# Performance work log

Hardware: AMD Instinct MI355X
Metric: run time of the kernel (lower is better)

Reference implementation:

```python
import jax, jax.numpy as jnp
import numpy as np

H_IMG, W_IMG = 256, 512      # image_size
P = 224                      # focus_patch_size
FS = 14                      # feature_size -> L = 196
DM = 384                     # d_model
POOL = P // FS               # 16


def _grid_sample_bilinear_zeros(img, grid):
    """torch F.grid_sample(mode='bilinear', padding_mode='zeros', align_corners=False).
    img: (B, C, H, W), grid: (B, Ho, Wo, 2) with (x, y) in [-1, 1]. -> (B, C, Ho, Wo)"""
    B, C, H, W = img.shape
    ix = (grid[..., 0] + 1.0) * (W * 0.5) - 0.5
    iy = (grid[..., 1] + 1.0) * (H * 0.5) - 0.5
    x0 = jnp.floor(ix); y0 = jnp.floor(iy)
    x1 = x0 + 1.0;      y1 = y0 + 1.0
    wx1 = ix - x0; wx0 = 1.0 - wx1
    wy1 = iy - y0; wy0 = 1.0 - wy1

    def gather(im, yy, xx):
        valid = ((xx >= 0) & (xx < W) & (yy >= 0) & (yy < H)).astype(im.dtype)
        xc = jnp.clip(xx, 0, W - 1).astype(jnp.int32)
        yc = jnp.clip(yy, 0, H - 1).astype(jnp.int32)
        return im[:, yc, xc] * valid[None]  # (C, Ho, Wo)

    def sample_one(im, x0, x1, y0, y1, wx0, wx1, wy0, wy1):
        return (gather(im, y0, x0) * (wy0 * wx0)[None]
                + gather(im, y0, x1) * (wy0 * wx1)[None]
                + gather(im, y1, x0) * (wy1 * wx0)[None]
                + gather(im, y1, x1) * (wy1 * wx1)[None])

    return jax.vmap(sample_one)(img, x0, x1, y0, y1, wx0, wx1, wy0, wy1)


def setup_inputs() -> dict:
    key = jax.random.key(0)
    ks = jax.random.split(key, 9)
    B = 128
    images = jax.random.normal(ks[0], (B, 3, H_IMG, W_IMG), jnp.float32)
    positions = jax.random.uniform(ks[1], (B, 2), jnp.float32)          # (x, y) in [0,1]
    global_features = jax.random.normal(ks[2], (B, FS * FS, DM), jnp.float32)
    Wp = jax.random.normal(ks[3], (3, DM), jnp.float32) * 0.1           # focus_net stand-in proj
    bp = jnp.zeros((DM,), jnp.float32)
    w1 = jax.random.normal(ks[4], (DM, DM // 4), jnp.float32) * 0.05    # fusion-weight MLP
    b1 = jnp.zeros((DM // 4,), jnp.float32)
    w2 = jax.random.normal(ks[5], (DM // 4, 1), jnp.float32) * 0.05
    b2 = jnp.zeros((1,), jnp.float32)
    return dict(images=images, positions=positions, global_features=global_features,
                Wp=Wp, bp=bp, w1=w1, b1=b1, w2=w2, b2=b2, seq_len=1)


def reference(images, positions, global_features, Wp, bp, w1, b1, w2, b2, seq_len):
    B = images.shape[0]
    L = FS * FS
    # ---- get_img_patches: wraparound crop (vectorized over batch) ----
    px = jnp.clip(positions[:, 0], 0.0, 1.0)
    py = jnp.clip(positions[:, 1], 0.0, 1.0)
    x_start = (jnp.trunc(px * W_IMG - P / 2).astype(jnp.int32)) % W_IMG           # int() then % W
    y_start = jnp.floor(jnp.clip(py * H_IMG - P / 2, 0.0, H_IMG - P)).astype(jnp.int32)
    xi = (x_start[:, None] + jnp.arange(P)[None, :]) % W_IMG                      # (B, P) wraparound
    yi = y_start[:, None] + jnp.arange(P)[None, :]                                # (B, P)
    patches = jax.vmap(lambda im, y, x: im[:, y][:, :, x])(images, yi, xi)        # (B, 3, P, P)

    # affine_grid(theta, (1,1,FS,FS), align_corners=False)
    xs = x_start.astype(jnp.float32)
    ys = y_start.astype(jnp.float32)
    u = ((jnp.arange(FS, dtype=jnp.float32) + 0.5) * 2.0 / FS) - 1.0              # base grid coords
    gx = (P / W_IMG) * u[None, None, :] + ((2.0 * xs + P) / W_IMG - 1.0)[:, None, None]
    gy = (P / H_IMG) * u[None, :, None] + ((2.0 * ys + P) / H_IMG - 1.0)[:, None, None]
    grid = jnp.stack([jnp.broadcast_to(gx, (B, FS, FS)),
                      jnp.broadcast_to(gy, (B, FS, FS))], axis=-1)                # (B, FS, FS, 2)

    # ---- focus_net stand-in: 16x16 avg-pool + linear 3 -> d_model ----
    pooled = patches.reshape(B, 3, FS, POOL, FS, POOL).mean(axis=(3, 5))          # (B, 3, FS, FS)
    local = jnp.einsum('bchw,cd->bhwd', pooled, Wp) + bp                          # (B, FS, FS, DM)
    local_features = local.reshape(B, L, DM)

    # ---- update_global_features: grid_sample scatter + gated update ----
    local_2d = local.transpose(0, 3, 1, 2)                                        # (B, DM, FS, FS)
    fw = jax.nn.sigmoid(jnp.einsum('blk,ko->blo',
                                   jax.nn.gelu(jnp.einsum('blc,ch->blh', local_features, w1) + b1),
                                   w2) + b2)                                      # (B, L, 1)
    sampled = _grid_sample_bilinear_zeros(local_2d, grid)                         # (B, DM, FS, FS)
    sampled = sampled.transpose(0, 2, 3, 1).reshape(B, L, DM)
    updated = global_features + fw * sampled                                      # broadcast expand
    return updated
```

## Files before the change

kernel.cpp:

```cpp
#include <hip/hip_runtime.h>
#include <math.h>

#define H_IMG 256
#define W_IMG 512
#define PSZ   224
#define FS    14
#define L     196
#define DM    384
#define HID   96

__device__ __forceinline__ void get_starts(const float* __restrict__ pos, int b,
                                           int& xs, int& ys) {
    float px = pos[b * 2 + 0];
    float py = pos[b * 2 + 1];
    px = fminf(fmaxf(px, 0.0f), 1.0f);
    py = fminf(fmaxf(py, 0.0f), 1.0f);
    int xv = (int)truncf(px * (float)W_IMG - 112.0f);
    xs = ((xv % W_IMG) + W_IMG) % W_IMG;
    float yv = py * (float)H_IMG - 112.0f;
    yv = fminf(fmaxf(yv, 0.0f), (float)(H_IMG - PSZ));
    ys = (int)floorf(yv);
}

__global__ __launch_bounds__(256) void pool_kernel(const float* __restrict__ img,
                                                   const float* __restrict__ pos,
                                                   float* __restrict__ pooled,
                                                   int B) {
    int blk = blockIdx.x;
    int b = blk / FS;
    int i = blk % FS;
    int t = threadIdx.x;
    int xs, ys;
    get_starts(pos, b, xs, ys);
    if (t < PSZ) {
        int col = xs + t;
        if (col >= W_IMG) col -= W_IMG;
        int row0 = ys + i * 16;
        #pragma unroll
        for (int c = 0; c < 3; ++c) {
            const float* ip = img + ((size_t)(b * 3 + c) * H_IMG) * W_IMG;
            float acc = 0.0f;
            #pragma unroll
            for (int dy = 0; dy < 16; ++dy)
                acc += ip[(size_t)(row0 + dy) * W_IMG + col];
            acc += __shfl_xor(acc, 1);
            acc += __shfl_xor(acc, 2);
            acc += __shfl_xor(acc, 4);
            acc += __shfl_xor(acc, 8);
            if ((t & 15) == 0)
                pooled[(size_t)(b * 3 + c) * L + i * FS + (t >> 4)] = acc * (1.0f / 256.0f);
        }
    }
}

__global__ void precompute_kernel(const float* __restrict__ Wp, const float* __restrict__ bp,
                                  const float* __restrict__ w1, const float* __restrict__ b1,
                                  float* __restrict__ A, float* __restrict__ B0) {
    int k = threadIdx.x;
    if (k < HID) {
        float a0 = 0.f, a1 = 0.f, a2 = 0.f, ab = 0.f;
        for (int d = 0; d < DM; ++d) {
            float w = w1[d * HID + k];
            a0 += Wp[0 * DM + d] * w;
            a1 += Wp[1 * DM + d] * w;
            a2 += Wp[2 * DM + d] * w;
            ab += bp[d] * w;
        }
        A[0 * HID + k] = a0;
        A[1 * HID + k] = a1;
        A[2 * HID + k] = a2;
        B0[k] = ab + b1[k];
    }
}

__global__ __launch_bounds__(256) void fw_kernel(const float* __restrict__ pos,
                                                 const float* __restrict__ pooled,
                                                 const float* __restrict__ A,
                                                 const float* __restrict__ B0,
                                                 const float* __restrict__ w2,
                                                 const float* __restrict__ b2,
                                                 float4* __restrict__ metaA,
                                                 float* __restrict__ metaB,
                                                 int B) {
    __shared__ float sA[3 * HID];
    __shared__ float sB0[HID];
    __shared__ float sw2[HID];
    for (int k = threadIdx.x; k < 3 * HID; k += blockDim.x) sA[k] = A[k];
    for (int k = threadIdx.x; k < HID; k += blockDim.x) { sB0[k] = B0[k]; sw2[k] = w2[k]; }
    __syncthreads();

    int idx = blockIdx.x * blockDim.x + threadIdx.x;
    if (idx >= B * L) return;
    int b = idx / L;
    int l = idx % L;
    int i = l / FS;
    int j = l % FS;

    const float* pb = pooled + (size_t)b * 3 * L;
    float p0 = pb[l], p1 = pb[L + l], p2 = pb[2 * L + l];

    float s = 0.0f;
    for (int k = 0; k < HID; ++k) {
        float x = sB0[k] + p0 * sA[k] + p1 * sA[HID + k] + p2 * sA[2 * HID + k];
        float inner = 0.7978845608028654f * (x + 0.044715f * x * x * x);
        float g = 0.5f * x * (1.0f + tanhf(inner));
        s += g * sw2[k];
    }
    float fw = 1.0f / (1.0f + expf(-(s + b2[0])));

    int xs, ys;
    get_starts(pos, b, xs, ys);
    float uj = ((j + 0.5f) * 2.0f) / 14.0f - 1.0f;
    float ui = ((i + 0.5f) * 2.0f) / 14.0f - 1.0f;
    float gx = (224.0f / 512.0f) * uj + ((2.0f * (float)xs + 224.0f) / 512.0f - 1.0f);
    float gy = (224.0f / 256.0f) * ui + ((2.0f * (float)ys + 224.0f) / 256.0f - 1.0f);
    float ix = (gx + 1.0f) * 7.0f - 0.5f;
    float iy = (gy + 1.0f) * 7.0f - 0.5f;
    float x0f = floorf(ix), y0f = floorf(iy);
    float wx1 = ix - x0f, wx0 = 1.0f - wx1;
    float wy1 = iy - y0f, wy0 = 1.0f - wy1;
    int x0 = (int)x0f, y0 = (int)y0f;
    int x1 = x0 + 1, y1 = y0 + 1;

    float ps0 = 0.f, ps1 = 0.f, ps2 = 0.f, wsum = 0.f;
    const int   cx[4] = { x0, x1, x0, x1 };
    const int   cy[4] = { y0, y0, y1, y1 };
    const float cw[4] = { wy0 * wx0, wy0 * wx1, wy1 * wx0, wy1 * wx1 };
    #pragma unroll
    for (int n = 0; n < 4; ++n) {
        int X = cx[n], Y = cy[n];
        if (X >= 0 && X < FS && Y >= 0 && Y < FS) {
            float w = cw[n];
            int li = Y * FS + X;
            ps0 += w * pb[li];
            ps1 += w * pb[L + li];
            ps2 += w * pb[2 * L + li];
            wsum += w;
        }
    }
    metaA[idx] = make_float4(fw, wsum, ps0, ps1);
    metaB[idx] = ps2;
}

__global__ __launch_bounds__(256) void update_kernel(const float* __restrict__ gf,
                                                     const float* __restrict__ Wp,
                                                     const float* __restrict__ bp,
                                                     const float4* __restrict__ metaA,
                                                     const float* __restrict__ metaB,
                                                     float* __restrict__ out,
                                                     int total4) {
    int idx4 = blockIdx.x * blockDim.x + threadIdx.x;
    if (idx4 >= total4) return;
    int token = idx4 / (DM / 4);
    int d4 = idx4 % (DM / 4);

    float4 m = metaA[token];
    float ps2 = metaB[token];
    float fw = m.x, wsum = m.y, ps0 = m.z, ps1 = m.w;

    const float4* gf4 = (const float4*)gf;
    const float4* Wp4 = (const float4*)Wp;
    const float4* bp4 = (const float4*)bp;
    float4 g  = gf4[idx4];
    float4 w0 = Wp4[0 * (DM / 4) + d4];
    float4 w1v = Wp4[1 * (DM / 4) + d4];
    float4 w2v = Wp4[2 * (DM / 4) + d4];
    float4 bv = bp4[d4];

    float4 o;
    o.x = g.x + fw * (wsum * bv.x + ps0 * w0.x + ps1 * w1v.x + ps2 * w2v.x);
    o.y = g.y + fw * (wsum * bv.y + ps0 * w0.y + ps1 * w1v.y + ps2 * w2v.y);
    o.z = g.z + fw * (wsum * bv.z + ps0 * w0.z + ps1 * w1v.z + ps2 * w2v.z);
    o.w = g.w + fw * (wsum * bv.w + ps0 * w0.w + ps1 * w1v.w + ps2 * w2v.w);
    ((float4*)out)[idx4] = o;
}

extern "C" void kernel_launch(void* const* d_in, const int* in_sizes, int n_in,
                              void* d_out, int out_size, void* d_ws, size_t ws_size,
                              hipStream_t stream) {
    const float* images    = (const float*)d_in[0];
    const float* positions = (const float*)d_in[1];
    const float* gf        = (const float*)d_in[2];
    const float* Wp        = (const float*)d_in[3];
    const float* bp        = (const float*)d_in[4];
    const float* w1        = (const float*)d_in[5];
    const float* b1        = (const float*)d_in[6];
    const float* w2        = (const float*)d_in[7];
    const float* b2        = (const float*)d_in[8];

    const int B = in_sizes[1] / 2;

    float* ws = (float*)d_ws;
    float*  pooled = ws;
    float*  A      = ws + (size_t)B * 3 * L;
    float*  B0     = A + 3 * HID;
    float*  metaAf = B0 + HID;
    float4* metaA  = (float4*)metaAf;
    float*  metaB  = metaAf + (size_t)B * L * 4;

    hipLaunchKernelGGL(pool_kernel, dim3(B * FS), dim3(256), 0, stream,
                       images, positions, pooled, B);
    hipLaunchKernelGGL(precompute_kernel, dim3(1), dim3(128), 0, stream,
                       Wp, bp, w1, b1, A, B0);
    int tok = B * L;
    hipLaunchKernelGGL(fw_kernel, dim3((tok + 255) / 256), dim3(256), 0, stream,
                       positions, pooled, A, B0, w2, b2, metaA, metaB, B);
    int total4 = tok * (DM / 4);
    hipLaunchKernelGGL(update_kernel, dim3((total4 + 255) / 256), dim3(256), 0, stream,
                       gf, Wp, bp, metaA, metaB, (float*)d_out, total4);
}
```

Measured before the change: 65.16 us.

## Fuse pooling with weight precompute and fw computation with the update

Merges the four launches into two. The tiny weight precompute now runs inside block 0 of the pooling kernel, and the per-token gate/sampling computation is fused into the broadcast update kernel through shared-memory metadata, so the metaA/metaB round trip through global memory goes away. The gate MLP is split across 8 threads per token using a fast exp-based tanh, and Wp/bp are staged in shared memory. Pooling now accumulates all three channels in one loop. The fast-math tanh changes numerics slightly, and the gate work per block adds latency before the streaming phase.

Result: faster. 59.91 us (-8.1%).

```diff
diff --git a/kernel.cpp b/kernel.cpp
--- a/kernel.cpp
+++ b/kernel.cpp
@@ -8,6 +8,7 @@
 #define L     196
 #define DM    384
 #define HID   96
+#define TPB   32
 
 __device__ __forceinline__ void get_starts(const float* __restrict__ pos, int b,
                                            int& xs, int& ys) {
@@ -22,157 +23,178 @@
     ys = (int)floorf(yv);
 }
 
-__global__ __launch_bounds__(256) void pool_kernel(const float* __restrict__ img,
-                                                   const float* __restrict__ pos,
-                                                   float* __restrict__ pooled,
-                                                   int B) {
+__global__ __launch_bounds__(256) void pool_pre_kernel(
+    const float* __restrict__ img, const float* __restrict__ pos,
+    const float* __restrict__ Wp,  const float* __restrict__ bp,
+    const float* __restrict__ w1,  const float* __restrict__ b1,
+    float* __restrict__ pooled, float* __restrict__ A, float* __restrict__ B0,
+    int B)
+{
+    const int HW = H_IMG * W_IMG;
     int blk = blockIdx.x;
     int b = blk / FS;
     int i = blk % FS;
     int t = threadIdx.x;
     int xs, ys;
     get_starts(pos, b, xs, ys);
+
     if (t < PSZ) {
         int col = xs + t;
         if (col >= W_IMG) col -= W_IMG;
         int row0 = ys + i * 16;
+        const float* ip = img + (size_t)b * 3 * HW + (size_t)row0 * W_IMG + col;
+        float a0 = 0.f, a1 = 0.f, a2 = 0.f;
         #pragma unroll
-        for (int c = 0; c < 3; ++c) {
-            const float* ip = img + ((size_t)(b * 3 + c) * H_IMG) * W_IMG;
-            float acc = 0.0f;
-            #pragma unroll
-            for (int dy = 0; dy < 16; ++dy)
-                acc += ip[(size_t)(row0 + dy) * W_IMG + col];
-            acc += __shfl_xor(acc, 1);
-            acc += __shfl_xor(acc, 2);
-            acc += __shfl_xor(acc, 4);
-            acc += __shfl_xor(acc, 8);
-            if ((t & 15) == 0)
-                pooled[(size_t)(b * 3 + c) * L + i * FS + (t >> 4)] = acc * (1.0f / 256.0f);
-        }
-    }
-}
-
-__global__ void precompute_kernel(const float* __restrict__ Wp, const float* __restrict__ bp,
-                                  const float* __restrict__ w1, const float* __restrict__ b1,
-                                  float* __restrict__ A, float* __restrict__ B0) {
-    int k = threadIdx.x;
-    if (k < HID) {
+        for (int dy = 0; dy < 16; ++dy) {
+            const float* r = ip + dy * W_IMG;
+            a0 += r[0];
+            a1 += r[HW];
+            a2 += r[2 * HW];
+        }
+        #pragma unroll
+        for (int d = 1; d < 16; d <<= 1) {
+            a0 += __shfl_xor(a0, d);
+            a1 += __shfl_xor(a1, d);
+            a2 += __shfl_xor(a2, d);
+        }
+        if ((t & 15) == 0) {
+            int li = i * FS + (t >> 4);
+            pooled[((size_t)b * 3 + 0) * L + li] = a0 * (1.0f / 256.0f);
+            pooled[((size_t)b * 3 + 1) * L + li] = a1 * (1.0f / 256.0f);
+            pooled[((size_t)b * 3 + 2) * L + li] = a2 * (1.0f / 256.0f);
+        }
+    }
+
+    if (blk == 0 && t < HID) {
         float a0 = 0.f, a1 = 0.f, a2 = 0.f, ab = 0.f;
+        #pragma unroll 4
         for (int d = 0; d < DM; ++d) {
-            float w = w1[d * HID + k];
+            float w = w1[d * HID + t];
             a0 += Wp[0 * DM + d] * w;
             a1 += Wp[1 * DM + d] * w;
             a2 += Wp[2 * DM + d] * w;
             ab += bp[d] * w;
         }
-        A[0 * HID + k] = a0;
-        A[1 * HID + k] = a1;
-        A[2 * HID + k] = a2;
-        B0[k] = ab + b1[k];
-    }
-}
-
-__global__ __launch_bounds__(256) void fw_kernel(const float* __restrict__ pos,
-                                                 const float* __restrict__ pooled,
-                                                 const float* __restrict__ A,
-                                                 const float* __restrict__ B0,
-                                                 const float* __restrict__ w2,
-                                                 const float* __restrict__ b2,
-                                                 float4* __restrict__ metaA,
-                                                 float* __restrict__ metaB,
-                                                 int B) {
-    __shared__ float sA[3 * HID];
-    __shared__ float sB0[HID];
-    __shared__ float sw2[HID];
-    for (int k = threadIdx.x; k < 3 * HID; k += blockDim.x) sA[k] = A[k];
-    for (int k = threadIdx.x; k < HID; k += blockDim.x) { sB0[k] = B0[k]; sw2[k] = w2[k]; }
+        A[0 * HID + t] = a0;
+        A[1 * HID + t] = a1;
+        A[2 * HID + t] = a2;
+        B0[t] = ab + b1[t];
+    }
+}
+
+__global__ __launch_bounds__(256) void fused_update_kernel(
+    const float* __restrict__ pos, const float* __restrict__ pooled,
+    const float* __restrict__ A,   const float* __restrict__ B0,
+    const float* __restrict__ w2,  const float* __restrict__ b2,
+    const float* __restrict__ gf,  const float* __restrict__ Wp,
+    const float* __restrict__ bp,  float* __restrict__ out, int B)
+{
+    __shared__ float  sA[3 * HID];
+    __shared__ float  sB0[HID];
+    __shared__ float  sw2[HID];
+    __shared__ float4 sWp4[3 * DM / 4];
+    __shared__ float4 sbp4[DM / 4];
+    __shared__ float  sMeta[TPB][5];
+
+    int tid = threadIdx.x;
+    if (tid < 3 * HID) sA[tid] = A[tid];
+    if (tid < HID) { sB0[tid] = B0[tid]; sw2[tid] = w2[tid]; }
+    {
+        if (tid < 288) sWp4[tid] = ((const float4*)Wp)[tid];
+        if (tid < 96)  sbp4[tid] = ((const float4*)bp)[tid];
+    }
     __syncthreads();
 
-    int idx = blockIdx.x * blockDim.x + threadIdx.x;
-    if (idx >= B * L) return;
-    int b = idx / L;
-    int l = idx % L;
-    int i = l / FS;
-    int j = l % FS;
+    const int nTok = B * L;
+    int bt = blockIdx.x * TPB;
+    int g = tid >> 3;
+    int s = tid & 7;
+    int token = bt + g;
+    if (token >= nTok) token = nTok - 1;
+    int b = token / L;
+    int l = token % L;
 
     const float* pb = pooled + (size_t)b * 3 * L;
     float p0 = pb[l], p1 = pb[L + l], p2 = pb[2 * L + l];
 
-    float s = 0.0f;
-    for (int k = 0; k < HID; ++k) {
+    float acc = 0.0f;
+    #pragma unroll
+    for (int m = 0; m < 12; ++m) {
+        int k = s + 8 * m;
         float x = sB0[k] + p0 * sA[k] + p1 * sA[HID + k] + p2 * sA[2 * HID + k];
-        float inner = 0.7978845608028654f * (x + 0.044715f * x * x * x);
-        float g = 0.5f * x * (1.0f + tanhf(inner));
-        s += g * sw2[k];
-    }
-    float fw = 1.0f / (1.0f + expf(-(s + b2[0])));
-
-    int xs, ys;
-    get_starts(pos, b, xs, ys);
-    float uj = ((j + 0.5f) * 2.0f) / 14.0f - 1.0f;
-    float ui = ((i + 0.5f) * 2.0f) / 14.0f - 1.0f;
-    float gx = (224.0f / 512.0f) * uj + ((2.0f * (float)xs + 224.0f) / 512.0f - 1.0f);
-    float gy = (224.0f / 256.0f) * ui + ((2.0f * (float)ys + 224.0f) / 256.0f - 1.0f);
-    float ix = (gx + 1.0f) * 7.0f - 0.5f;
-    float iy = (gy + 1.0f) * 7.0f - 0.5f;
-    float x0f = floorf(ix), y0f = floorf(iy);
-    float wx1 = ix - x0f, wx0 = 1.0f - wx1;
-    float wy1 = iy - y0f, wy0 = 1.0f - wy1;
-    int x0 = (int)x0f, y0 = (int)y0f;
-    int x1 = x0 + 1, y1 = y0 + 1;
-
-    float ps0 = 0.f, ps1 = 0.f, ps2 = 0.f, wsum = 0.f;
-    const int   cx[4] = { x0, x1, x0, x1 };
-    const int   cy[4] = { y0, y0, y1, y1 };
-    const float cw[4] = { wy0 * wx0, wy0 * wx1, wy1 * wx0, wy1 * wx1 };
+        float e = __expf(1.5957691216057308f * (x + 0.044715f * x * x * x));
+        float th = 1.0f - 2.0f / (e + 1.0f);
+        acc += 0.5f * x * (1.0f + th) * sw2[k];
+    }
+    acc += __shfl_xor(acc, 1);
+    acc += __shfl_xor(acc, 2);
+    acc += __shfl_xor(acc, 4);
+
+    if (s == 0) {
+        float fw = 1.0f / (1.0f + __expf(-(acc + b2[0])));
+
+        int xs, ys;
+        get_starts(pos, b, xs, ys);
+        int i = l / FS, j = l % FS;
+        float uj = ((j + 0.5f) * 2.0f) / 14.0f - 1.0f;
+        float ui = ((i + 0.5f) * 2.0f) / 14.0f - 1.0f;
+        float gx = (224.0f / 512.0f) * uj + ((2.0f * (float)xs + 224.0f) / 512.0f - 1.0f);
+        float gy = (224.0f / 256.0f) * ui + ((2.0f * (float)ys + 224.0f) / 256.0f - 1.0f);
+        float ix = (gx + 1.0f) * 7.0f - 0.5f;
+        float iy = (gy + 1.0f) * 7.0f - 0.5f;
+        float x0f = floorf(ix), y0f = floorf(iy);
+        float wx1 = ix - x0f, wx0 = 1.0f - wx1;
+        float wy1 = iy - y0f, wy0 = 1.0f - wy1;
+        int x0 = (int)x0f, y0 = (int)y0f;
+        int x1 = x0 + 1, y1 = y0 + 1;
+
+        float ps0 = 0.f, ps1 = 0.f, ps2 = 0.f, wsum = 0.f;
+        const int   cx[4] = { x0, x1, x0, x1 };
+        const int   cy[4] = { y0, y0, y1, y1 };
+        const float cw[4] = { wy0 * wx0, wy0 * wx1, wy1 * wx0, wy1 * wx1 };
+        #pragma unroll
+        for (int n = 0; n < 4; ++n) {
+            int X = cx[n], Y = cy[n];
+            if (X >= 0 && X < FS && Y >= 0 && Y < FS) {
+                float w = cw[n];
+                int li = Y * FS + X;
+                ps0 += w * pb[li];
+                ps1 += w * pb[L + li];
+                ps2 += w * pb[2 * L + li];
+                wsum += w;
+            }
+        }
+        sMeta[g][0] = fw;  sMeta[g][1] = wsum;
+        sMeta[g][2] = ps0; sMeta[g][3] = ps1; sMeta[g][4] = ps2;
+    }
+    __syncthreads();
+
+    const float4* gf4  = (const float4*)gf  + (size_t)bt * (DM / 4);
+    float4*       out4 = (float4*)out       + (size_t)bt * (DM / 4);
+    long long maxItem = (long long)(nTok - bt) * (DM / 4);
     #pragma unroll
-    for (int n = 0; n < 4; ++n) {
-        int X = cx[n], Y = cy[n];
-        if (X >= 0 && X < FS && Y >= 0 && Y < FS) {
-            float w = cw[n];
-            int li = Y * FS + X;
-            ps0 += w * pb[li];
-            ps1 += w * pb[L + li];
-            ps2 += w * pb[2 * L + li];
-            wsum += w;
-        }
-    }
-    metaA[idx] = make_float4(fw, wsum, ps0, ps1);
-    metaB[idx] = ps2;
-}
-
-__global__ __launch_bounds__(256) void update_kernel(const float* __restrict__ gf,
-                                                     const float* __restrict__ Wp,
-                                                     const float* __restrict__ bp,
-                                                     const float4* __restrict__ metaA,
-                                                     const float* __restrict__ metaB,
-                                                     float* __restrict__ out,
-                                                     int total4) {
-    int idx4 = blockIdx.x * blockDim.x + threadIdx.x;
-    if (idx4 >= total4) return;
-    int token = idx4 / (DM / 4);
-    int d4 = idx4 % (DM / 4);
-
-    float4 m = metaA[token];
-    float ps2 = metaB[token];
-    float fw = m.x, wsum = m.y, ps0 = m.z, ps1 = m.w;
-
-    const float4* gf4 = (const float4*)gf;
-    const float4* Wp4 = (const float4*)Wp;
-    const float4* bp4 = (const float4*)bp;
-    float4 g  = gf4[idx4];
-    float4 w0 = Wp4[0 * (DM / 4) + d4];
-    float4 w1v = Wp4[1 * (DM / 4) + d4];
-    float4 w2v = Wp4[2 * (DM / 4) + d4];
-    float4 bv = bp4[d4];
-
-    float4 o;
-    o.x = g.x + fw * (wsum * bv.x + ps0 * w0.x + ps1 * w1v.x + ps2 * w2v.x);
-    o.y = g.y + fw * (wsum * bv.y + ps0 * w0.y + ps1 * w1v.y + ps2 * w2v.y);
-    o.z = g.z + fw * (wsum * bv.z + ps0 * w0.z + ps1 * w1v.z + ps2 * w2v.z);
-    o.w = g.w + fw * (wsum * bv.w + ps0 * w0.w + ps1 * w1v.w + ps2 * w2v.w);
-    ((float4*)out)[idx4] = o;
+    for (int it = 0; it < 12; ++it) {
+        int item = it * 256 + tid;
+        if (item >= maxItem) break;
+        int tl = item / (DM / 4);
+        int d4 = item - tl * (DM / 4);
+        float fw   = sMeta[tl][0];
+        float wsum = sMeta[tl][1];
+        float ps0  = sMeta[tl][2];
+        float ps1  = sMeta[tl][3];
+        float ps2  = sMeta[tl][4];
+        float4 g4 = gf4[item];
+        float4 w0 = sWp4[d4];
+        float4 w1v = sWp4[96 + d4];
+        float4 w2v = sWp4[192 + d4];
+        float4 bv = sbp4[d4];
+        float4 o;
+        o.x = g4.x + fw * (wsum * bv.x + ps0 * w0.x + ps1 * w1v.x + ps2 * w2v.x);
+        o.y = g4.y + fw * (wsum * bv.y + ps0 * w0.y + ps1 * w1v.y + ps2 * w2v.y);
+        o.z = g4.z + fw * (wsum * bv.z + ps0 * w0.z + ps1 * w1v.z + ps2 * w2v.z);
+        o.w = g4.w + fw * (wsum * bv.w + ps0 * w0.w + ps1 * w1v.w + ps2 * w2v.w);
+        out4[item] = o;
+    }
 }
 
 extern "C" void kernel_launch(void* const* d_in, const int* in_sizes, int n_in,
@@ -191,21 +213,14 @@
     const int B = in_sizes[1] / 2;
 
     float* ws = (float*)d_ws;
-    float*  pooled = ws;
-    float*  A      = ws + (size_t)B * 3 * L;
-    float*  B0     = A + 3 * HID;
-    float*  metaAf = B0 + HID;
-    float4* metaA  = (float4*)metaAf;
-    float*  metaB  = metaAf + (size_t)B * L * 4;
-
-    hipLaunchKernelGGL(pool_kernel, dim3(B * FS), dim3(256), 0, stream,
-                       images, positions, pooled, B);
-    hipLaunchKernelGGL(precompute_kernel, dim3(1), dim3(128), 0, stream,
-                       Wp, bp, w1, b1, A, B0);
-    int tok = B * L;
-    hipLaunchKernelGGL(fw_kernel, dim3((tok + 255) / 256), dim3(256), 0, stream,
-                       positions, pooled, A, B0, w2, b2, metaA, metaB, B);
-    int total4 = tok * (DM / 4);
-    hipLaunchKernelGGL(update_kernel, dim3((total4 + 255) / 256), dim3(256), 0, stream,
-                       gf, Wp, bp, metaA, metaB, (float*)d_out, total4);
-}
+    float* pooled = ws;
+    float* A      = ws + (size_t)B * 3 * L;
+    float* B0     = A + 3 * HID;
+
+    hipLaunchKernelGGL(pool_pre_kernel, dim3(B * FS), dim3(256), 0, stream,
+                       images, positions, Wp, bp, w1, b1, pooled, A, B0, B);
+
+    int nTok = B * L;
+    hipLaunchKernelGGL(fused_update_kernel, dim3((nTok + TPB - 1) / TPB), dim3(256), 0, stream,
+                       positions, pooled, A, B0, w2, b2, gf, Wp, bp, (float*)d_out, B);
+}
```
